# Optimization experiments

Measured on AMD Instinct MI355X. Metric: run time of the kernel, lower is better.

The kernel has to match this reference:

```python
import jax, jax.numpy as jnp
import numpy as np

H = 128          # hidden_size
L = 3            # num_layers
N = 200_000      # total atoms across all fragments
E = 400_000      # bidirectional bonds (avg degree ~2)
G = 8192         # number of molecular subgraphs
ATOM_V = 120
BOND_V = 5


def setup_inputs() -> dict:
    key = jax.random.key(0)
    ks = jax.random.split(key, 14)
    s = 1.0 / np.sqrt(H)
    f = lambda k, shp: (jax.random.normal(k, shp, jnp.float32) * s)
    return {
        "atom_types": jax.random.randint(ks[0], (N,), 0, ATOM_V),
        "edges": jax.random.randint(ks[1], (2, E), 0, N),
        "edge_types": jax.random.randint(ks[2], (E,), 0, BOND_V),
        "node_batch": jnp.sort(jax.random.randint(ks[3], (N,), 0, G)),
        "atom_emb": f(ks[4], (ATOM_V, H)),
        "bond_emb": f(ks[5], (BOND_V, H)),
        "conv_w1": f(ks[6], (L, H, H)),
        "conv_b1": jnp.zeros((L, H), jnp.float32),
        "conv_w2": f(ks[7], (L, H, H)),
        "conv_b2": jnp.zeros((L, H), jnp.float32),
        "proj_w1": f(ks[8], (H, H)),
        "proj_b1": jnp.zeros((H,), jnp.float32),
        "proj_w2": f(ks[9], (H, H)),
        "proj_b2": jnp.zeros((H,), jnp.float32),
    }


def reference(atom_types, edges, edge_types, node_batch,
              atom_emb, bond_emb,
              conv_w1, conv_b1, conv_w2, conv_b2,
              proj_w1, proj_b1, proj_w2, proj_b2):
    # node / bond embeddings (torch clamps indices to vocab-1)
    x = atom_emb[jnp.clip(atom_types, 0, ATOM_V - 1)]       # [N, H]
    a = bond_emb[jnp.clip(edge_types, 0, BOND_V - 1)]       # [E, H]
    src, dst = edges[0], edges[1]
    # GINEConv layers: x_i' = MLP(x_i + sum_{j->i} ReLU(x_j + e_ji)), eps=0
    for l in range(L):
        m = jax.nn.relu(x[src] + a)                         # [E, H] edge messages
        agg = jax.ops.segment_sum(m, dst, num_segments=N)   # scatter-add to dst nodes
        h = x + agg
        h = jax.nn.relu(h @ conv_w1[l] + conv_b1[l])
        x = h @ conv_w2[l] + conv_b2[l]
    # per-graph mean readout
    sums = jax.ops.segment_sum(x, node_batch, num_segments=G)                      # [G, H]
    cnt = jax.ops.segment_sum(jnp.ones((N, 1), x.dtype), node_batch, num_segments=G)
    g = sums / jnp.maximum(cnt, 1.0)
    # proj: Linear -> SiLU -> Linear
    g = jax.nn.silu(g @ proj_w1 + proj_b1)
    return g @ proj_w2 + proj_b2                            # [G, H]
```

## Files before the change

### kernel.cpp

```cpp
#include <hip/hip_runtime.h>

typedef unsigned short u16;
typedef __attribute__((ext_vector_type(8))) short short8;
typedef __attribute__((ext_vector_type(4))) float f32x4;

#define HDIM 128
#define SCAN_B 512
#define CSH 2048
#define PREP_BLOCKS 572

__device__ __forceinline__ float bf2f(u16 v) {
    return __uint_as_float(((unsigned int)v) << 16);
}
__device__ __forceinline__ u16 f2bf(float f) {
    unsigned int u = __float_as_uint(f);
    unsigned int r = (u + 0x7FFFu + ((u >> 16) & 1u)) >> 16;
    return (u16)r;
}

__global__ __launch_bounds__(256) void prep_hist_kernel(
    const float* __restrict__ w1, const float* __restrict__ w2,
    const float* __restrict__ pw1, const float* __restrict__ pw2,
    const float* __restrict__ atom_emb,
    u16* __restrict__ wt, u16* __restrict__ ebf,
    const int* __restrict__ edges, int* __restrict__ deg, int E, int N)
{
    if (blockIdx.x < PREP_BLOCKS) {
        int gid = blockIdx.x * 256 + threadIdx.x;
        if (gid < 8 * 16384) {
            int mat = gid >> 14;
            int idx = gid & 16383;
            int n = idx >> 7, k = idx & 127;
            const float* src;
            if      (mat < 3) src = w1 + mat * 16384;
            else if (mat < 6) src = w2 + (mat - 3) * 16384;
            else if (mat == 6) src = pw1;
            else               src = pw2;
            wt[gid] = f2bf(src[k * 128 + n]);
        } else {
            int i = gid - 8 * 16384;
            ebf[i] = f2bf(atom_emb[i]);
        }
    } else {
        int e = (blockIdx.x - PREP_BLOCKS) * 256 + threadIdx.x;
        if (e >= E) return;
        int d = edges[E + e];
        d = d < 0 ? 0 : (d >= N ? N - 1 : d);
        atomicAdd(&deg[d], 1);
    }
}

__global__ __launch_bounds__(SCAN_B) void scan_block_kernel(
    const int* __restrict__ deg, int* __restrict__ offs, int* __restrict__ bsum, int N)
{
    __shared__ int tmp[SCAN_B];
    int t = threadIdx.x;
    int gid = blockIdx.x * SCAN_B + t;
    int v = (gid < N) ? deg[gid] : 0;
    tmp[t] = v;
    __syncthreads();
#pragma unroll
    for (int off = 1; off < SCAN_B; off <<= 1) {
        int add = (t >= off) ? tmp[t - off] : 0;
        __syncthreads();
        tmp[t] += add;
        __syncthreads();
    }
    if (gid < N) offs[gid] = tmp[t] - v;
    if (t == SCAN_B - 1) bsum[blockIdx.x] = tmp[t];
}

__global__ __launch_bounds__(256) void finalize_offs_kernel(
    int* __restrict__ offs, const int* __restrict__ bsum,
    int* __restrict__ cursor, const int* __restrict__ nb,
    int* __restrict__ gbounds, int N, int E, int G)
{
    __shared__ int red[256];
    const int tid = threadIdx.x;
    const int B = blockIdx.x >> 1;
    int sum = 0;
    for (int t = tid; t < B; t += 256) sum += bsum[t];
    red[tid] = sum;
    __syncthreads();
#pragma unroll
    for (int off = 128; off > 0; off >>= 1) {
        if (tid < off) red[tid] += red[tid + off];
        __syncthreads();
    }
    int prefix = red[0];
    int gid = blockIdx.x * 256 + tid;
    if (gid < N) {
        int v = offs[gid] + prefix;
        offs[gid] = v;
        cursor[gid] = v;
        int cur = nb[gid]; cur = cur < 0 ? 0 : (cur > G - 1 ? G - 1 : cur);
        if (gid == 0) {
            for (int g = 0; g <= cur; g++) gbounds[g] = 0;
        } else {
            int prev = nb[gid - 1]; prev = prev < 0 ? 0 : (prev > G - 1 ? G - 1 : prev);
            for (int g = prev + 1; g <= cur; g++) gbounds[g] = gid;
        }
        if (gid == N - 1) {
            for (int g = cur + 1; g <= G; g++) gbounds[g] = N;
        }
    }
    if (gid == 0) offs[N] = E;
}

__global__ __launch_bounds__(256) void fill_csr_kernel(
    const int* __restrict__ edges, const int* __restrict__ etypes,
    int* __restrict__ cursor, int* __restrict__ csr, int E, int N)
{
    int e = blockIdx.x * 256 + threadIdx.x;
    if (e >= E) return;
    int s = edges[e], d = edges[E + e], t = etypes[e];
    s = s < 0 ? 0 : (s >= N ? N - 1 : s);
    d = d < 0 ? 0 : (d >= N ? N - 1 : d);
    t = t < 0 ? 0 : (t > 4 ? 4 : t);
    int pos = atomicAdd(&cursor[d], 1);
    csr[pos] = (s << 3) | t;
}

__global__ __launch_bounds__(512, 4) void gine_kernel(
    const u16* __restrict__ x_in, u16* __restrict__ x_out,
    const int* __restrict__ types, int use_emb, const u16* __restrict__ ebf,
    const int* __restrict__ offs, const int* __restrict__ csr,
    const float* __restrict__ bond_emb,
    const u16* __restrict__ w1t, const float* __restrict__ b1,
    const u16* __restrict__ w2t, const float* __restrict__ b2, int N)
{
    __shared__ __align__(16) u16 As[128][136];
    __shared__ __align__(16) u16 Ws[128][136];
    __shared__ __align__(16) u16 bsh[5 * 128];
    __shared__ __align__(16) int csh[CSH];
    const int tid  = threadIdx.x;
    const int row0 = blockIdx.x * 128;
    const int wave = tid >> 6, lane = tid & 63;
    const int m = lane & 15, quad = lane >> 4;

    for (int i = tid; i < 640; i += 512) bsh[i] = f2bf(bond_emb[i]);
    {
        const uint4* src = (const uint4*)w1t;
        for (int i = tid; i < 2048; i += 512) {
            int n = i >> 4, k8 = i & 15;
            *(uint4*)&Ws[n][k8 * 8] = src[i];
        }
    }
    const int rend = (row0 + 128 < N) ? row0 + 128 : N;
    const int e0 = offs[row0];
    {
        int cnt = offs[rend] - e0;
        cnt = cnt < CSH ? cnt : CSH;
        for (int i = tid; i < cnt; i += 512) csh[i] = csr[e0 + i];
    }
    {
        const int rp = tid >> 4, c8 = (tid & 15) * 8;
        __syncthreads();

        int rowA = row0 + rp,      rowB = row0 + 32 + rp;
        int rowC = row0 + 64 + rp, rowD = row0 + 96 + rp;
        int rcA = rowA < N ? rowA : N - 1;
        int rcB = rowB < N ? rowB : N - 1;
        int rcC = rowC < N ? rowC : N - 1;
        int rcD = rowD < N ? rowD : N - 1;
        const u16 *spA, *spB, *spC, *spD;
        if (use_emb) {
            int tA = types[rcA]; tA = tA < 0 ? 0 : (tA > 119 ? 119 : tA);
            int tB = types[rcB]; tB = tB < 0 ? 0 : (tB > 119 ? 119 : tB);
            int tC = types[rcC]; tC = tC < 0 ? 0 : (tC > 119 ? 119 : tC);
            int tD = types[rcD]; tD = tD < 0 ? 0 : (tD > 119 ? 119 : tD);
            spA = ebf + (size_t)tA * 128; spB = ebf + (size_t)tB * 128;
            spC = ebf + (size_t)tC * 128; spD = ebf + (size_t)tD * 128;
        } else {
            spA = x_in + (size_t)rcA * 128; spB = x_in + (size_t)rcB * 128;
            spC = x_in + (size_t)rcC * 128; spD = x_in + (size_t)rcD * 128;
        }
        int jbA = offs[rcA], jeA = rowA < N ? offs[rcA + 1] : jbA;
        int jbB = offs[rcB], jeB = rowB < N ? offs[rcB + 1] : jbB;
        int jbC = offs[rcC], jeC = rowC < N ? offs[rcC + 1] : jbC;
        int jbD = offs[rcD], jeD = rowD < N ? offs[rcD + 1] : jbD;
        uint4 svA = *(const uint4*)(spA + c8);
        uint4 svB = *(const uint4*)(spB + c8);
        uint4 svC = *(const uint4*)(spC + c8);
        uint4 svD = *(const uint4*)(spD + c8);
        float accA[8], accB[8], accC[8], accD[8];
        {
            const u16* pA = (const u16*)&svA; const u16* pB = (const u16*)&svB;
            const u16* pC = (const u16*)&svC; const u16* pD = (const u16*)&svD;
#pragma unroll
            for (int i = 0; i < 8; i++) {
                accA[i] = bf2f(pA[i]); accB[i] = bf2f(pB[i]);
                accC[i] = bf2f(pC[i]); accD[i] = bf2f(pD[i]);
            }
        }
        int lbA = jbA - e0, lbB = jbB - e0, lbC = jbC - e0, lbD = jbD - e0;
        int dA = jeA - jbA, dB = jeB - jbB, dC = jeC - jbC, dD = jeD - jbD;
        int dmax = dA > dB ? dA : dB;
        dmax = dC > dmax ? dC : dmax;
        dmax = dD > dmax ? dD : dmax;
        for (int k = 0; k < dmax; k += 2) {
            bool a0 = k < dA,     a1 = (k + 1) < dA;
            bool a2 = k < dB,     a3 = (k + 1) < dB;
            bool a4 = k < dC,     a5 = (k + 1) < dC;
            bool a6 = k < dD,     a7 = (k + 1) < dD;
            int v0 = 0, v1 = 0, v2 = 0, v3 = 0, v4 = 0, v5 = 0, v6 = 0, v7 = 0;
            if (a0) { int li = lbA + k;     v0 = (li < CSH) ? csh[li] : csr[jbA + k]; }
            if (a1) { int li = lbA + k + 1; v1 = (li < CSH) ? csh[li] : csr[jbA + k + 1]; }
            if (a2) { int li = lbB + k;     v2 = (li < CSH) ? csh[li] : csr[jbB + k]; }
            if (a3) { int li = lbB + k + 1; v3 = (li < CSH) ? csh[li] : csr[jbB + k + 1]; }
            if (a4) { int li = lbC + k;     v4 = (li < CSH) ? csh[li] : csr[jbC + k]; }
            if (a5) { int li = lbC + k + 1; v5 = (li < CSH) ? csh[li] : csr[jbC + k + 1]; }
            if (a6) { int li = lbD + k;     v6 = (li < CSH) ? csh[li] : csr[jbD + k]; }
            if (a7) { int li = lbD + k + 1; v7 = (li < CSH) ? csh[li] : csr[jbD + k + 1]; }
            const u16 *p0, *p1, *p2, *p3, *p4, *p5, *p6, *p7;
            if (use_emb) {
                int t0 = types[v0 >> 3]; t0 = t0 < 0 ? 0 : (t0 > 119 ? 119 : t0);
                int t1 = types[v1 >> 3]; t1 = t1 < 0 ? 0 : (t1 > 119 ? 119 : t1);
                int t2 = types[v2 >> 3]; t2 = t2 < 0 ? 0 : (t2 > 119 ? 119 : t2);
                int t3 = types[v3 >> 3]; t3 = t3 < 0 ? 0 : (t3 > 119 ? 119 : t3);
                int t4 = types[v4 >> 3]; t4 = t4 < 0 ? 0 : (t4 > 119 ? 119 : t4);
                int t5 = types[v5 >> 3]; t5 = t5 < 0 ? 0 : (t5 > 119 ? 119 : t5);
                int t6 = types[v6 >> 3]; t6 = t6 < 0 ? 0 : (t6 > 119 ? 119 : t6);
                int t7 = types[v7 >> 3]; t7 = t7 < 0 ? 0 : (t7 > 119 ? 119 : t7);
                p0 = ebf + (size_t)t0 * 128; p1 = ebf + (size_t)t1 * 128;
                p2 = ebf + (size_t)t2 * 128; p3 = ebf + (size_t)t3 * 128;
                p4 = ebf + (size_t)t4 * 128; p5 = ebf + (size_t)t5 * 128;
                p6 = ebf + (size_t)t6 * 128; p7 = ebf + (size_t)t7 * 128;
            } else {
                p0 = x_in + (size_t)(v0 >> 3) * 128; p1 = x_in + (size_t)(v1 >> 3) * 128;
                p2 = x_in + (size_t)(v2 >> 3) * 128; p3 = x_in + (size_t)(v3 >> 3) * 128;
                p4 = x_in + (size_t)(v4 >> 3) * 128; p5 = x_in + (size_t)(v5 >> 3) * 128;
                p6 = x_in + (size_t)(v6 >> 3) * 128; p7 = x_in + (size_t)(v7 >> 3) * 128;
            }
            uint4 g0 = *(const uint4*)(p0 + c8);
            uint4 g1 = *(const uint4*)(p1 + c8);
            uint4 g2 = *(const uint4*)(p2 + c8);
            uint4 g3 = *(const uint4*)(p3 + c8);
            uint4 g4 = *(const uint4*)(p4 + c8);
            uint4 g5 = *(const uint4*)(p5 + c8);
            uint4 g6 = *(const uint4*)(p6 + c8);
            uint4 g7 = *(const uint4*)(p7 + c8);
            if (a0) { const u16* gp = (const u16*)&g0; const u16* bp = bsh + (v0 & 7) * 128 + c8;
#pragma unroll
                for (int i = 0; i < 8; i++) { float mm = bf2f(gp[i]) + bf2f(bp[i]); accA[i] += mm > 0.f ? mm : 0.f; } }
            if (a1) { const u16* gp = (const u16*)&g1; const u16* bp = bsh + (v1 & 7) * 128 + c8;
#pragma unroll
                for (int i = 0; i < 8; i++) { float mm = bf2f(gp[i]) + bf2f(bp[i]); accA[i] += mm > 0.f ? mm : 0.f; } }
            if (a2) { const u16* gp = (const u16*)&g2; const u16* bp = bsh + (v2 & 7) * 128 + c8;
#pragma unroll
                for (int i = 0; i < 8; i++) { float mm = bf2f(gp[i]) + bf2f(bp[i]); accB[i] += mm > 0.f ? mm : 0.f; } }
            if (a3) { const u16* gp = (const u16*)&g3; const u16* bp = bsh + (v3 & 7) * 128 + c8;
#pragma unroll
                for (int i = 0; i < 8; i++) { float mm = bf2f(gp[i]) + bf2f(bp[i]); accB[i] += mm > 0.f ? mm : 0.f; } }
            if (a4) { const u16* gp = (const u16*)&g4; const u16* bp = bsh + (v4 & 7) * 128 + c8;
#pragma unroll
                for (int i = 0; i < 8; i++) { float mm = bf2f(gp[i]) + bf2f(bp[i]); accC[i] += mm > 0.f ? mm : 0.f; } }
            if (a5) { const u16* gp = (const u16*)&g5; const u16* bp = bsh + (v5 & 7) * 128 + c8;
#pragma unroll
                for (int i = 0; i < 8; i++) { float mm = bf2f(gp[i]) + bf2f(bp[i]); accC[i] += mm > 0.f ? mm : 0.f; } }
            if (a6) { const u16* gp = (const u16*)&g6; const u16* bp = bsh + (v6 & 7) * 128 + c8;
#pragma unroll
                for (int i = 0; i < 8; i++) { float mm = bf2f(gp[i]) + bf2f(bp[i]); accD[i] += mm > 0.f ? mm : 0.f; } }
            if (a7) { const u16* gp = (const u16*)&g7; const u16* bp = bsh + (v7 & 7) * 128 + c8;
#pragma unroll
                for (int i = 0; i < 8; i++) { float mm = bf2f(gp[i]) + bf2f(bp[i]); accD[i] += mm > 0.f ? mm : 0.f; } }
        }
        uint4 ovA = make_uint4(0u,0u,0u,0u), ovB = ovA, ovC = ovA, ovD = ovA;
        if (rowA < N) { u16* op = (u16*)&ovA;
#pragma unroll
            for (int i = 0; i < 8; i++) op[i] = f2bf(accA[i]); }
        if (rowB < N) { u16* op = (u16*)&ovB;
#pragma unroll
            for (int i = 0; i < 8; i++) op[i] = f2bf(accB[i]); }
        if (rowC < N) { u16* op = (u16*)&ovC;
#pragma unroll
            for (int i = 0; i < 8; i++) op[i] = f2bf(accC[i]); }
        if (rowD < N) { u16* op = (u16*)&ovD;
#pragma unroll
            for (int i = 0; i < 8; i++) op[i] = f2bf(accD[i]); }
        *(uint4*)&As[rp][c8]      = ovA;
        *(uint4*)&As[32 + rp][c8] = ovB;
        *(uint4*)&As[64 + rp][c8] = ovC;
        *(uint4*)&As[96 + rp][c8] = ovD;
    }
    __syncthreads();

    f32x4 acc[8];
#pragma unroll
    for (int c = 0; c < 8; c++) acc[c] = (f32x4){0.f, 0.f, 0.f, 0.f};
#pragma unroll
    for (int q = 0; q < 4; q++) {
        short8 a = *(const short8*)&As[wave * 16 + m][q * 32 + quad * 8];
#pragma unroll
        for (int c = 0; c < 8; c++) {
            short8 b = *(const short8*)&Ws[c * 16 + m][q * 32 + quad * 8];
            acc[c] = __builtin_amdgcn_mfma_f32_16x16x32_bf16(a, b, acc[c], 0, 0, 0);
        }
    }
    __syncthreads();
    {
        const uint4* src = (const uint4*)w2t;
        for (int i = tid; i < 2048; i += 512) {
            int n = i >> 4, k8 = i & 15;
            *(uint4*)&Ws[n][k8 * 8] = src[i];
        }
    }
#pragma unroll
    for (int c = 0; c < 8; c++) {
        int col = c * 16 + m;
        float bias = b1[col];
#pragma unroll
        for (int r = 0; r < 4; r++) {
            float v = acc[c][r] + bias;
            v = v > 0.f ? v : 0.f;
            As[wave * 16 + quad * 4 + r][col] = f2bf(v);
        }
    }
    __syncthreads();
    f32x4 acc2[8];
#pragma unroll
    for (int c = 0; c < 8; c++) acc2[c] = (f32x4){0.f, 0.f, 0.f, 0.f};
#pragma unroll
    for (int q = 0; q < 4; q++) {
        short8 a = *(const short8*)&As[wave * 16 + m][q * 32 + quad * 8];
#pragma unroll
        for (int c = 0; c < 8; c++) {
            short8 b = *(const short8*)&Ws[c * 16 + m][q * 32 + quad * 8];
            acc2[c] = __builtin_amdgcn_mfma_f32_16x16x32_bf16(a, b, acc2[c], 0, 0, 0);
        }
    }
    __syncthreads();
#pragma unroll
    for (int c = 0; c < 8; c++) {
        int col = c * 16 + m;
        float bias = b2[col];
#pragma unroll
        for (int r = 0; r < 4; r++)
            As[wave * 16 + quad * 4 + r][col] = f2bf(acc2[c][r] + bias);
    }
    __syncthreads();
    for (int i = tid; i < 2048; i += 512) {
        int r = i >> 4, c8 = (i & 15) * 8;
        int row = row0 + r;
        if (row < N) *(uint4*)(x_out + (size_t)row * 128 + c8) = *(const uint4*)&As[r][c8];
    }
}

__global__ __launch_bounds__(256) void readout_mean_kernel(
    const u16* __restrict__ x, const int* __restrict__ gbounds,
    u16* __restrict__ gm, int N)
{
    __shared__ float part[16][128];
    int b = blockIdx.x;
    int tid = threadIdx.x;
    int s = gbounds[b], e = gbounds[b + 1];
    int rg = tid >> 4, c8 = (tid & 15) * 8;
    float acc[8];
#pragma unroll
    for (int i = 0; i < 8; i++) acc[i] = 0.f;
    for (int n = s + rg; n < e; n += 16) {
        uint4 v = *(const uint4*)(x + (size_t)n * 128 + c8);
        const u16* vp = (const u16*)&v;
#pragma unroll
        for (int i = 0; i < 8; i++) acc[i] += bf2f(vp[i]);
    }
#pragma unroll
    for (int i = 0; i < 8; i++) part[rg][c8 + i] = acc[i];
    __syncthreads();
    if (tid < 128) {
        float sum = 0.f;
#pragma unroll
        for (int g = 0; g < 16; g++) sum += part[g][tid];
        float cnt = (float)((e - s) > 0 ? (e - s) : 1);
        gm[(size_t)b * 128 + tid] = f2bf(sum / cnt);
    }
}

__global__ __launch_bounds__(256) void proj_kernel(
    const u16* __restrict__ gm, float* __restrict__ out,
    const u16* __restrict__ pw1t, const float* __restrict__ pb1,
    const u16* __restrict__ pw2t, const float* __restrict__ pb2, int G)
{
    __shared__ __align__(16) u16 As[64][136];
    __shared__ __align__(16) u16 Ws[128][136];
    const int tid  = threadIdx.x;
    const int row0 = blockIdx.x * 64;
    const int wave = tid >> 6, lane = tid & 63;
    const int m = lane & 15, quad = lane >> 4;

    {
        const uint4* src = (const uint4*)pw1t;
        for (int i = tid; i < 2048; i += 256) {
            int n = i >> 4, k8 = i & 15;
            *(uint4*)&Ws[n][k8 * 8] = src[i];
        }
    }
    for (int i = tid; i < 1024; i += 256) {
        int r = i >> 4, c8 = (i & 15) * 8;
        int row = row0 + r;
        uint4 ov = make_uint4(0u, 0u, 0u, 0u);
        if (row < G) ov = *(const uint4*)(gm + (size_t)row * 128 + c8);
        *(uint4*)&As[r][c8] = ov;
    }
    __syncthreads();
    f32x4 acc[8];
#pragma unroll
    for (int c = 0; c < 8; c++) acc[c] = (f32x4){0.f, 0.f, 0.f, 0.f};
#pragma unroll
    for (int q = 0; q < 4; q++) {
        short8 a = *(const short8*)&As[wave * 16 + m][q * 32 + quad * 8];
#pragma unroll
        for (int c = 0; c < 8; c++) {
            short8 b = *(const short8*)&Ws[c * 16 + m][q * 32 + quad * 8];
            acc[c] = __builtin_amdgcn_mfma_f32_16x16x32_bf16(a, b, acc[c], 0, 0, 0);
        }
    }
    __syncthreads();
    {
        const uint4* src = (const uint4*)pw2t;
        for (int i = tid; i < 2048; i += 256) {
            int n = i >> 4, k8 = i & 15;
            *(uint4*)&Ws[n][k8 * 8] = src[i];
        }
    }
#pragma unroll
    for (int c = 0; c < 8; c++) {
        int col = c * 16 + m;
        float bias = pb1[col];
#pragma unroll
        for (int r = 0; r < 4; r++) {
            float v = acc[c][r] + bias;
            v = v / (1.f + __expf(-v));
            As[wave * 16 + quad * 4 + r][col] = f2bf(v);
        }
    }
    __syncthreads();
    f32x4 acc2[8];
#pragma unroll
    for (int c = 0; c < 8; c++) acc2[c] = (f32x4){0.f, 0.f, 0.f, 0.f};
#pragma unroll
    for (int q = 0; q < 4; q++) {
        short8 a = *(const short8*)&As[wave * 16 + m][q * 32 + quad * 8];
#pragma unroll
        for (int c = 0; c < 8; c++) {
            short8 b = *(const short8*)&Ws[c * 16 + m][q * 32 + quad * 8];
            acc2[c] = __builtin_amdgcn_mfma_f32_16x16x32_bf16(a, b, acc2[c], 0, 0, 0);
        }
    }
#pragma unroll
    for (int c = 0; c < 8; c++) {
        int col = c * 16 + m;
        float bias = pb2[col];
#pragma unroll
        for (int r = 0; r < 4; r++) {
            int row = row0 + wave * 16 + quad * 4 + r;
            if (row < G) out[(size_t)row * 128 + col] = acc2[c][r] + bias;
        }
    }
}

extern "C" void kernel_launch(void* const* d_in, const int* in_sizes, int n_in,
                              void* d_out, int out_size, void* d_ws, size_t ws_size,
                              hipStream_t stream) {
    const int*   atom_types  = (const int*)d_in[0];
    const int*   edges       = (const int*)d_in[1];
    const int*   edge_types  = (const int*)d_in[2];
    const int*   node_batch  = (const int*)d_in[3];
    const float* atom_emb    = (const float*)d_in[4];
    const float* bond_emb    = (const float*)d_in[5];
    const float* conv_w1     = (const float*)d_in[6];
    const float* conv_b1     = (const float*)d_in[7];
    const float* conv_w2     = (const float*)d_in[8];
    const float* conv_b2     = (const float*)d_in[9];
    const float* pw1         = (const float*)d_in[10];
    const float* pb1         = (const float*)d_in[11];
    const float* pw2         = (const float*)d_in[12];
    const float* pb2         = (const float*)d_in[13];
    float* out = (float*)d_out;

    const int N = in_sizes[0];
    const int E = in_sizes[2];
    const int G = out_size / HDIM;
    const int nblk = (N + SCAN_B - 1) / SCAN_B;

    size_t xA_bytes  = (size_t)N * HDIM * sizeof(u16);
    size_t xB_bytes  = (size_t)N * HDIM * sizeof(u16);
    size_t wt_bytes  = (size_t)8 * HDIM * HDIM * sizeof(u16);
    size_t ebf_bytes = (size_t)120 * HDIM * sizeof(u16);
    size_t gm_bytes  = (size_t)G * HDIM * sizeof(u16);
    size_t deg_bytes = (size_t)N * 4;
    size_t off_bytes = (size_t)(N + 1) * 4;
    size_t cur_bytes = (size_t)N * 4;
    size_t bs_bytes  = (size_t)nblk * 4;
    size_t gb_bytes  = (size_t)(G + 1) * 4;
    size_t csr_bytes = (size_t)E * 4;
    size_t need = xA_bytes + xB_bytes + wt_bytes + ebf_bytes + gm_bytes +
                  deg_bytes + off_bytes + cur_bytes + bs_bytes + gb_bytes + csr_bytes;
    if (ws_size < need) {
        hipMemsetAsync(d_out, 0, (size_t)out_size * sizeof(float), stream);
        return;
    }
    char* p = (char*)d_ws;
    u16* xA     = (u16*)p;  p += xA_bytes;
    u16* xB     = (u16*)p;  p += xB_bytes;
    u16* wt     = (u16*)p;  p += wt_bytes;
    u16* ebf    = (u16*)p;  p += ebf_bytes;
    u16* gm     = (u16*)p;  p += gm_bytes;
    int* deg    = (int*)p;  p += deg_bytes;
    int* offs   = (int*)p;  p += off_bytes;
    int* cur    = (int*)p;  p += cur_bytes;
    int* bsum   = (int*)p;  p += bs_bytes;
    int* gbound = (int*)p;  p += gb_bytes;
    int* csr    = (int*)p;

    hipMemsetAsync(deg, 0, deg_bytes, stream);
    prep_hist_kernel<<<PREP_BLOCKS + (E + 255) / 256, 256, 0, stream>>>(
        conv_w1, conv_w2, pw1, pw2, atom_emb, wt, ebf, edges, deg, E, N);
    scan_block_kernel<<<nblk, SCAN_B, 0, stream>>>(deg, offs, bsum, N);
    finalize_offs_kernel<<<(N + 255) / 256, 256, 0, stream>>>(
        offs, bsum, cur, node_batch, gbound, N, E, G);
    fill_csr_kernel<<<(E + 255) / 256, 256, 0, stream>>>(edges, edge_types, cur, csr, E, N);

    const int gblocks = (N + 127) / 128;
    gine_kernel<<<gblocks, 512, 0, stream>>>(
        xB , xA, atom_types, 1, ebf, offs, csr, bond_emb,
        wt + 0 * 16384, conv_b1 + 0, wt + 3 * 16384, conv_b2 + 0, N);
    gine_kernel<<<gblocks, 512, 0, stream>>>(
        xA, xB, atom_types, 0, ebf, offs, csr, bond_emb,
        wt + 1 * 16384, conv_b1 + 128, wt + 4 * 16384, conv_b2 + 128, N);
    gine_kernel<<<gblocks, 512, 0, stream>>>(
        xB, xA, atom_types, 0, ebf, offs, csr, bond_emb,
        wt + 2 * 16384, conv_b1 + 256, wt + 5 * 16384, conv_b2 + 256, N);

    readout_mean_kernel<<<G, 256, 0, stream>>>(xA, gbound, gm, N);
    proj_kernel<<<(G + 63) / 64, 256, 0, stream>>>(
        gm, out, wt + 6 * 16384, pb1, wt + 7 * 16384, pb2, G);
}
```

Baseline: 342.4 us.

## Split fused GINE layer into separate aggregation and MLP kernels

The fused gather+MLP kernel is split into an aggregation kernel with small shared memory and launch bounds allowing 8 blocks per CU, plus a separate MFMA MLP kernel that reloads the aggregated rows from global memory. The shared-memory staging of the CSR slice is also dropped, so neighbour indices are read straight from global memory. The aim is higher occupancy for the latency-bound gather phase. In exchange there are extra kernel launches and an extra write and read of an N×128 bf16 intermediate per layer.

New measurement: 570.9 us. 66.7% more time.

```diff
diff --git a/kernel.cpp b/kernel.cpp
--- a/kernel.cpp
+++ b/kernel.cpp
@@ -6,7 +6,6 @@
 
 #define HDIM 128
 #define SCAN_B 512
-#define CSH 2048
 #define PREP_BLOCKS 572
 
 __device__ __forceinline__ float bf2f(u16 v) {
@@ -121,24 +120,155 @@
     csr[pos] = (s << 3) | t;
 }
 
-__global__ __launch_bounds__(512, 4) void gine_kernel(
-    const u16* __restrict__ x_in, u16* __restrict__ x_out,
+__global__ __launch_bounds__(512, 8) void agg_kernel(
+    const u16* __restrict__ x_in, u16* __restrict__ xa,
     const int* __restrict__ types, int use_emb, const u16* __restrict__ ebf,
     const int* __restrict__ offs, const int* __restrict__ csr,
-    const float* __restrict__ bond_emb,
+    const float* __restrict__ bond_emb, int N)
+{
+    __shared__ __align__(16) u16 bsh[5 * 128];
+    const int tid  = threadIdx.x;
+    const int row0 = blockIdx.x * 128;
+    for (int i = tid; i < 640; i += 512) bsh[i] = f2bf(bond_emb[i]);
+    const int rp = tid >> 4, c8 = (tid & 15) * 8;
+    __syncthreads();
+
+    int rowA = row0 + rp,      rowB = row0 + 32 + rp;
+    int rowC = row0 + 64 + rp, rowD = row0 + 96 + rp;
+    int rcA = rowA < N ? rowA : N - 1;
+    int rcB = rowB < N ? rowB : N - 1;
+    int rcC = rowC < N ? rowC : N - 1;
+    int rcD = rowD < N ? rowD : N - 1;
+    const u16 *spA, *spB, *spC, *spD;
+    if (use_emb) {
+        int tA = types[rcA]; tA = tA < 0 ? 0 : (tA > 119 ? 119 : tA);
+        int tB = types[rcB]; tB = tB < 0 ? 0 : (tB > 119 ? 119 : tB);
+        int tC = types[rcC]; tC = tC < 0 ? 0 : (tC > 119 ? 119 : tC);
+        int tD = types[rcD]; tD = tD < 0 ? 0 : (tD > 119 ? 119 : tD);
+        spA = ebf + (size_t)tA * 128; spB = ebf + (size_t)tB * 128;
+        spC = ebf + (size_t)tC * 128; spD = ebf + (size_t)tD * 128;
+    } else {
+        spA = x_in + (size_t)rcA * 128; spB = x_in + (size_t)rcB * 128;
+        spC = x_in + (size_t)rcC * 128; spD = x_in + (size_t)rcD * 128;
+    }
+    int jbA = offs[rcA], jeA = rowA < N ? offs[rcA + 1] : jbA;
+    int jbB = offs[rcB], jeB = rowB < N ? offs[rcB + 1] : jbB;
+    int jbC = offs[rcC], jeC = rowC < N ? offs[rcC + 1] : jbC;
+    int jbD = offs[rcD], jeD = rowD < N ? offs[rcD + 1] : jbD;
+    uint4 svA = *(const uint4*)(spA + c8);
+    uint4 svB = *(const uint4*)(spB + c8);
+    uint4 svC = *(const uint4*)(spC + c8);
+    uint4 svD = *(const uint4*)(spD + c8);
+    float accA[8], accB[8], accC[8], accD[8];
+    {
+        const u16* pA = (const u16*)&svA; const u16* pB = (const u16*)&svB;
+        const u16* pC = (const u16*)&svC; const u16* pD = (const u16*)&svD;
+#pragma unroll
+        for (int i = 0; i < 8; i++) {
+            accA[i] = bf2f(pA[i]); accB[i] = bf2f(pB[i]);
+            accC[i] = bf2f(pC[i]); accD[i] = bf2f(pD[i]);
+        }
+    }
+    int dA = jeA - jbA, dB = jeB - jbB, dC = jeC - jbC, dD = jeD - jbD;
+    int dmax = dA > dB ? dA : dB;
+    dmax = dC > dmax ? dC : dmax;
+    dmax = dD > dmax ? dD : dmax;
+    for (int k = 0; k < dmax; k += 2) {
+        bool a0 = k < dA,     a1 = (k + 1) < dA;
+        bool a2 = k < dB,     a3 = (k + 1) < dB;
+        bool a4 = k < dC,     a5 = (k + 1) < dC;
+        bool a6 = k < dD,     a7 = (k + 1) < dD;
+        int v0 = a0 ? csr[jbA + k] : 0;  int v1 = a1 ? csr[jbA + k + 1] : 0;
+        int v2 = a2 ? csr[jbB + k] : 0;  int v3 = a3 ? csr[jbB + k + 1] : 0;
+        int v4 = a4 ? csr[jbC + k] : 0;  int v5 = a5 ? csr[jbC + k + 1] : 0;
+        int v6 = a6 ? csr[jbD + k] : 0;  int v7 = a7 ? csr[jbD + k + 1] : 0;
+        const u16 *p0, *p1, *p2, *p3, *p4, *p5, *p6, *p7;
+        if (use_emb) {
+            int t0 = types[v0 >> 3]; t0 = t0 < 0 ? 0 : (t0 > 119 ? 119 : t0);
+            int t1 = types[v1 >> 3]; t1 = t1 < 0 ? 0 : (t1 > 119 ? 119 : t1);
+            int t2 = types[v2 >> 3]; t2 = t2 < 0 ? 0 : (t2 > 119 ? 119 : t2);
+            int t3 = types[v3 >> 3]; t3 = t3 < 0 ? 0 : (t3 > 119 ? 119 : t3);
+            int t4 = types[v4 >> 3]; t4 = t4 < 0 ? 0 : (t4 > 119 ? 119 : t4);
+            int t5 = types[v5 >> 3]; t5 = t5 < 0 ? 0 : (t5 > 119 ? 119 : t5);
+            int t6 = types[v6 >> 3]; t6 = t6 < 0 ? 0 : (t6 > 119 ? 119 : t6);
+            int t7 = types[v7 >> 3]; t7 = t7 < 0 ? 0 : (t7 > 119 ? 119 : t7);
+            p0 = ebf + (size_t)t0 * 128; p1 = ebf + (size_t)t1 * 128;
+            p2 = ebf + (size_t)t2 * 128; p3 = ebf + (size_t)t3 * 128;
+            p4 = ebf + (size_t)t4 * 128; p5 = ebf + (size_t)t5 * 128;
+            p6 = ebf + (size_t)t6 * 128; p7 = ebf + (size_t)t7 * 128;
+        } else {
+            p0 = x_in + (size_t)(v0 >> 3) * 128; p1 = x_in + (size_t)(v1 >> 3) * 128;
+            p2 = x_in + (size_t)(v2 >> 3) * 128; p3 = x_in + (size_t)(v3 >> 3) * 128;
+            p4 = x_in + (size_t)(v4 >> 3) * 128; p5 = x_in + (size_t)(v5 >> 3) * 128;
+            p6 = x_in + (size_t)(v6 >> 3) * 128; p7 = x_in + (size_t)(v7 >> 3) * 128;
+        }
+        uint4 g0 = *(const uint4*)(p0 + c8);
+        uint4 g1 = *(const uint4*)(p1 + c8);
+        uint4 g2 = *(const uint4*)(p2 + c8);
+        uint4 g3 = *(const uint4*)(p3 + c8);
+        uint4 g4 = *(const uint4*)(p4 + c8);
+        uint4 g5 = *(const uint4*)(p5 + c8);
+        uint4 g6 = *(const uint4*)(p6 + c8);
+        uint4 g7 = *(const uint4*)(p7 + c8);
+        if (a0) { const u16* gp = (const u16*)&g0; const u16* bp = bsh + (v0 & 7) * 128 + c8;
+#pragma unroll
+            for (int i = 0; i < 8; i++) { float mm = bf2f(gp[i]) + bf2f(bp[i]); accA[i] += mm > 0.f ? mm : 0.f; } }
+        if (a1) { const u16* gp = (const u16*)&g1; const u16* bp = bsh + (v1 & 7) * 128 + c8;
+#pragma unroll
+            for (int i = 0; i < 8; i++) { float mm = bf2f(gp[i]) + bf2f(bp[i]); accA[i] += mm > 0.f ? mm : 0.f; } }
+        if (a2) { const u16* gp = (const u16*)&g2; const u16* bp = bsh + (v2 & 7) * 128 + c8;
+#pragma unroll
+            for (int i = 0; i < 8; i++) { float mm = bf2f(gp[i]) + bf2f(bp[i]); accB[i] += mm > 0.f ? mm : 0.f; } }
+        if (a3) { const u16* gp = (const u16*)&g3; const u16* bp = bsh + (v3 & 7) * 128 + c8;
+#pragma unroll
+            for (int i = 0; i < 8; i++) { float mm = bf2f(gp[i]) + bf2f(bp[i]); accB[i] += mm > 0.f ? mm : 0.f; } }
+        if (a4) { const u16* gp = (const u16*)&g4; const u16* bp = bsh + (v4 & 7) * 128 + c8;
+#pragma unroll
+            for (int i = 0; i < 8; i++) { float mm = bf2f(gp[i]) + bf2f(bp[i]); accC[i] += mm > 0.f ? mm : 0.f; } }
+        if (a5) { const u16* gp = (const u16*)&g5; const u16* bp = bsh + (v5 & 7) * 128 + c8;
+#pragma unroll
+            for (int i = 0; i < 8; i++) { float mm = bf2f(gp[i]) + bf2f(bp[i]); accC[i] += mm > 0.f ? mm : 0.f; } }
+        if (a6) { const u16* gp = (const u16*)&g6; const u16* bp = bsh + (v6 & 7) * 128 + c8;
+#pragma unroll
+            for (int i = 0; i < 8; i++) { float mm = bf2f(gp[i]) + bf2f(bp[i]); accD[i] += mm > 0.f ? mm : 0.f; } }
+        if (a7) { const u16* gp = (const u16*)&g7; const u16* bp = bsh + (v7 & 7) * 128 + c8;
+#pragma unroll
+            for (int i = 0; i < 8; i++) { float mm = bf2f(gp[i]) + bf2f(bp[i]); accD[i] += mm > 0.f ? mm : 0.f; } }
+    }
+    uint4 ovA, ovB, ovC, ovD;
+    {
+        u16* op;
+        op = (u16*)&ovA;
+#pragma unroll
+        for (int i = 0; i < 8; i++) op[i] = f2bf(accA[i]);
+        op = (u16*)&ovB;
+#pragma unroll
+        for (int i = 0; i < 8; i++) op[i] = f2bf(accB[i]);
+        op = (u16*)&ovC;
+#pragma unroll
+        for (int i = 0; i < 8; i++) op[i] = f2bf(accC[i]);
+        op = (u16*)&ovD;
+#pragma unroll
+        for (int i = 0; i < 8; i++) op[i] = f2bf(accD[i]);
+    }
+    if (rowA < N) *(uint4*)(xa + (size_t)rowA * 128 + c8) = ovA;
+    if (rowB < N) *(uint4*)(xa + (size_t)rowB * 128 + c8) = ovB;
+    if (rowC < N) *(uint4*)(xa + (size_t)rowC * 128 + c8) = ovC;
+    if (rowD < N) *(uint4*)(xa + (size_t)rowD * 128 + c8) = ovD;
+}
+
+__global__ __launch_bounds__(512, 4) void mlp_kernel(
+    const u16* __restrict__ xa, u16* __restrict__ x_out,
     const u16* __restrict__ w1t, const float* __restrict__ b1,
     const u16* __restrict__ w2t, const float* __restrict__ b2, int N)
 {
     __shared__ __align__(16) u16 As[128][136];
     __shared__ __align__(16) u16 Ws[128][136];
-    __shared__ __align__(16) u16 bsh[5 * 128];
-    __shared__ __align__(16) int csh[CSH];
     const int tid  = threadIdx.x;
     const int row0 = blockIdx.x * 128;
     const int wave = tid >> 6, lane = tid & 63;
     const int m = lane & 15, quad = lane >> 4;
 
-    for (int i = tid; i < 640; i += 512) bsh[i] = f2bf(bond_emb[i]);
     {
         const uint4* src = (const uint4*)w1t;
         for (int i = tid; i < 2048; i += 512) {
@@ -146,142 +276,12 @@
             *(uint4*)&Ws[n][k8 * 8] = src[i];
         }
     }
-    const int rend = (row0 + 128 < N) ? row0 + 128 : N;
-    const int e0 = offs[row0];
-    {
-        int cnt = offs[rend] - e0;
-        cnt = cnt < CSH ? cnt : CSH;
-        for (int i = tid; i < cnt; i += 512) csh[i] = csr[e0 + i];
-    }
-    {
-        const int rp = tid >> 4, c8 = (tid & 15) * 8;
-        __syncthreads();
-
-        int rowA = row0 + rp,      rowB = row0 + 32 + rp;
-        int rowC = row0 + 64 + rp, rowD = row0 + 96 + rp;
-        int rcA = rowA < N ? rowA : N - 1;
-        int rcB = rowB < N ? rowB : N - 1;
-        int rcC = rowC < N ? rowC : N - 1;
-        int rcD = rowD < N ? rowD : N - 1;
-        const u16 *spA, *spB, *spC, *spD;
-        if (use_emb) {
-            int tA = types[rcA]; tA = tA < 0 ? 0 : (tA > 119 ? 119 : tA);
-            int tB = types[rcB]; tB = tB < 0 ? 0 : (tB > 119 ? 119 : tB);
-            int tC = types[rcC]; tC = tC < 0 ? 0 : (tC > 119 ? 119 : tC);
-            int tD = types[rcD]; tD = tD < 0 ? 0 : (tD > 119 ? 119 : tD);
-            spA = ebf + (size_t)tA * 128; spB = ebf + (size_t)tB * 128;
-            spC = ebf + (size_t)tC * 128; spD = ebf + (size_t)tD * 128;
-        } else {
-            spA = x_in + (size_t)rcA * 128; spB = x_in + (size_t)rcB * 128;
-            spC = x_in + (size_t)rcC * 128; spD = x_in + (size_t)rcD * 128;
-        }
-        int jbA = offs[rcA], jeA = rowA < N ? offs[rcA + 1] : jbA;
-        int jbB = offs[rcB], jeB = rowB < N ? offs[rcB + 1] : jbB;
-        int jbC = offs[rcC], jeC = rowC < N ? offs[rcC + 1] : jbC;
-        int jbD = offs[rcD], jeD = rowD < N ? offs[rcD + 1] : jbD;
-        uint4 svA = *(const uint4*)(spA + c8);
-        uint4 svB = *(const uint4*)(spB + c8);
-        uint4 svC = *(const uint4*)(spC + c8);
-        uint4 svD = *(const uint4*)(spD + c8);
-        float accA[8], accB[8], accC[8], accD[8];
-        {
-            const u16* pA = (const u16*)&svA; const u16* pB = (const u16*)&svB;
-            const u16* pC = (const u16*)&svC; const u16* pD = (const u16*)&svD;
-#pragma unroll
-            for (int i = 0; i < 8; i++) {
-                accA[i] = bf2f(pA[i]); accB[i] = bf2f(pB[i]);
-                accC[i] = bf2f(pC[i]); accD[i] = bf2f(pD[i]);
-            }
-        }
-        int lbA = jbA - e0, lbB = jbB - e0, lbC = jbC - e0, lbD = jbD - e0;
-        int dA = jeA - jbA, dB = jeB - jbB, dC = jeC - jbC, dD = jeD - jbD;
-        int dmax = dA > dB ? dA : dB;
-        dmax = dC > dmax ? dC : dmax;
-        dmax = dD > dmax ? dD : dmax;
-        for (int k = 0; k < dmax; k += 2) {
-            bool a0 = k < dA,     a1 = (k + 1) < dA;
-            bool a2 = k < dB,     a3 = (k + 1) < dB;
-            bool a4 = k < dC,     a5 = (k + 1) < dC;
-            bool a6 = k < dD,     a7 = (k + 1) < dD;
-            int v0 = 0, v1 = 0, v2 = 0, v3 = 0, v4 = 0, v5 = 0, v6 = 0, v7 = 0;
-            if (a0) { int li = lbA + k;     v0 = (li < CSH) ? csh[li] : csr[jbA + k]; }
-            if (a1) { int li = lbA + k + 1; v1 = (li < CSH) ? csh[li] : csr[jbA + k + 1]; }
-            if (a2) { int li = lbB + k;     v2 = (li < CSH) ? csh[li] : csr[jbB + k]; }
-            if (a3) { int li = lbB + k + 1; v3 = (li < CSH) ? csh[li] : csr[jbB + k + 1]; }
-            if (a4) { int li = lbC + k;     v4 = (li < CSH) ? csh[li] : csr[jbC + k]; }
-            if (a5) { int li = lbC + k + 1; v5 = (li < CSH) ? csh[li] : csr[jbC + k + 1]; }
-            if (a6) { int li = lbD + k;     v6 = (li < CSH) ? csh[li] : csr[jbD + k]; }
-            if (a7) { int li = lbD + k + 1; v7 = (li < CSH) ? csh[li] : csr[jbD + k + 1]; }
-            const u16 *p0, *p1, *p2, *p3, *p4, *p5, *p6, *p7;
-            if (use_emb) {
-                int t0 = types[v0 >> 3]; t0 = t0 < 0 ? 0 : (t0 > 119 ? 119 : t0);
-                int t1 = types[v1 >> 3]; t1 = t1 < 0 ? 0 : (t1 > 119 ? 119 : t1);
-                int t2 = types[v2 >> 3]; t2 = t2 < 0 ? 0 : (t2 > 119 ? 119 : t2);
-                int t3 = types[v3 >> 3]; t3 = t3 < 0 ? 0 : (t3 > 119 ? 119 : t3);
-                int t4 = types[v4 >> 3]; t4 = t4 < 0 ? 0 : (t4 > 119 ? 119 : t4);
-                int t5 = types[v5 >> 3]; t5 = t5 < 0 ? 0 : (t5 > 119 ? 119 : t5);
-                int t6 = types[v6 >> 3]; t6 = t6 < 0 ? 0 : (t6 > 119 ? 119 : t6);
-                int t7 = types[v7 >> 3]; t7 = t7 < 0 ? 0 : (t7 > 119 ? 119 : t7);
-                p0 = ebf + (size_t)t0 * 128; p1 = ebf + (size_t)t1 * 128;
-                p2 = ebf + (size_t)t2 * 128; p3 = ebf + (size_t)t3 * 128;
-                p4 = ebf + (size_t)t4 * 128; p5 = ebf + (size_t)t5 * 128;
-                p6 = ebf + (size_t)t6 * 128; p7 = ebf + (size_t)t7 * 128;
-            } else {
-                p0 = x_in + (size_t)(v0 >> 3) * 128; p1 = x_in + (size_t)(v1 >> 3) * 128;
-                p2 = x_in + (size_t)(v2 >> 3) * 128; p3 = x_in + (size_t)(v3 >> 3) * 128;
-                p4 = x_in + (size_t)(v4 >> 3) * 128; p5 = x_in + (size_t)(v5 >> 3) * 128;
-                p6 = x_in + (size_t)(v6 >> 3) * 128; p7 = x_in + (size_t)(v7 >> 3) * 128;
-            }
-            uint4 g0 = *(const uint4*)(p0 + c8);
-            uint4 g1 = *(const uint4*)(p1 + c8);
-            uint4 g2 = *(const uint4*)(p2 + c8);
-            uint4 g3 = *(const uint4*)(p3 + c8);
-            uint4 g4 = *(const uint4*)(p4 + c8);
-            uint4 g5 = *(const uint4*)(p5 + c8);
-            uint4 g6 = *(const uint4*)(p6 + c8);
-            uint4 g7 = *(const uint4*)(p7 + c8);
-            if (a0) { const u16* gp = (const u16*)&g0; const u16* bp = bsh + (v0 & 7) * 128 + c8;
-#pragma unroll
-                for (int i = 0; i < 8; i++) { float mm = bf2f(gp[i]) + bf2f(bp[i]); accA[i] += mm > 0.f ? mm : 0.f; } }
-            if (a1) { const u16* gp = (const u16*)&g1; const u16* bp = bsh + (v1 & 7) * 128 + c8;
-#pragma unroll
-                for (int i = 0; i < 8; i++) { float mm = bf2f(gp[i]) + bf2f(bp[i]); accA[i] += mm > 0.f ? mm : 0.f; } }
-            if (a2) { const u16* gp = (const u16*)&g2; const u16* bp = bsh + (v2 & 7) * 128 + c8;
-#pragma unroll
-                for (int i = 0; i < 8; i++) { float mm = bf2f(gp[i]) + bf2f(bp[i]); accB[i] += mm > 0.f ? mm : 0.f; } }
-            if (a3) { const u16* gp = (const u16*)&g3; const u16* bp = bsh + (v3 & 7) * 128 + c8;
-#pragma unroll
-                for (int i = 0; i < 8; i++) { float mm = bf2f(gp[i]) + bf2f(bp[i]); accB[i] += mm > 0.f ? mm : 0.f; } }
-            if (a4) { const u16* gp = (const u16*)&g4; const u16* bp = bsh + (v4 & 7) * 128 + c8;
-#pragma unroll
-                for (int i = 0; i < 8; i++) { float mm = bf2f(gp[i]) + bf2f(bp[i]); accC[i] += mm > 0.f ? mm : 0.f; } }
-            if (a5) { const u16* gp = (const u16*)&g5; const u16* bp = bsh + (v5 & 7) * 128 + c8;
-#pragma unroll
-                for (int i = 0; i < 8; i++) { float mm = bf2f(gp[i]) + bf2f(bp[i]); accC[i] += mm > 0.f ? mm : 0.f; } }
-            if (a6) { const u16* gp = (const u16*)&g6; const u16* bp = bsh + (v6 & 7) * 128 + c8;
-#pragma unroll
-                for (int i = 0; i < 8; i++) { float mm = bf2f(gp[i]) + bf2f(bp[i]); accD[i] += mm > 0.f ? mm : 0.f; } }
-            if (a7) { const u16* gp = (const u16*)&g7; const u16* bp = bsh + (v7 & 7) * 128 + c8;
-#pragma unroll
-                for (int i = 0; i < 8; i++) { float mm = bf2f(gp[i]) + bf2f(bp[i]); accD[i] += mm > 0.f ? mm : 0.f; } }
-        }
-        uint4 ovA = make_uint4(0u,0u,0u,0u), ovB = ovA, ovC = ovA, ovD = ovA;
-        if (rowA < N) { u16* op = (u16*)&ovA;
-#pragma unroll
-            for (int i = 0; i < 8; i++) op[i] = f2bf(accA[i]); }
-        if (rowB < N) { u16* op = (u16*)&ovB;
-#pragma unroll
-            for (int i = 0; i < 8; i++) op[i] = f2bf(accB[i]); }
-        if (rowC < N) { u16* op = (u16*)&ovC;
-#pragma unroll
-            for (int i = 0; i < 8; i++) op[i] = f2bf(accC[i]); }
-        if (rowD < N) { u16* op = (u16*)&ovD;
-#pragma unroll
-            for (int i = 0; i < 8; i++) op[i] = f2bf(accD[i]); }
-        *(uint4*)&As[rp][c8]      = ovA;
-        *(uint4*)&As[32 + rp][c8] = ovB;
-        *(uint4*)&As[64 + rp][c8] = ovC;
-        *(uint4*)&As[96 + rp][c8] = ovD;
+    for (int i = tid; i < 2048; i += 512) {
+        int r = i >> 4, c8 = (i & 15) * 8;
+        int row = row0 + r;
+        uint4 ov = make_uint4(0u, 0u, 0u, 0u);
+        if (row < N) ov = *(const uint4*)(xa + (size_t)row * 128 + c8);
+        *(uint4*)&As[r][c8] = ov;
     }
     __syncthreads();
 
@@ -522,15 +522,18 @@
     fill_csr_kernel<<<(E + 255) / 256, 256, 0, stream>>>(edges, edge_types, cur, csr, E, N);
 
     const int gblocks = (N + 127) / 128;
-    gine_kernel<<<gblocks, 512, 0, stream>>>(
-        xB , xA, atom_types, 1, ebf, offs, csr, bond_emb,
-        wt + 0 * 16384, conv_b1 + 0, wt + 3 * 16384, conv_b2 + 0, N);
-    gine_kernel<<<gblocks, 512, 0, stream>>>(
-        xA, xB, atom_types, 0, ebf, offs, csr, bond_emb,
-        wt + 1 * 16384, conv_b1 + 128, wt + 4 * 16384, conv_b2 + 128, N);
-    gine_kernel<<<gblocks, 512, 0, stream>>>(
-        xB, xA, atom_types, 0, ebf, offs, csr, bond_emb,
-        wt + 2 * 16384, conv_b1 + 256, wt + 5 * 16384, conv_b2 + 256, N);
+    agg_kernel<<<gblocks, 512, 0, stream>>>(
+        xA , xB, atom_types, 1, ebf, offs, csr, bond_emb, N);
+    mlp_kernel<<<gblocks, 512, 0, stream>>>(
+        xB, xA, wt + 0 * 16384, conv_b1 + 0, wt + 3 * 16384, conv_b2 + 0, N);
+    agg_kernel<<<gblocks, 512, 0, stream>>>(
+        xA, xB, atom_types, 0, ebf, offs, csr, bond_emb, N);
+    mlp_kernel<<<gblocks, 512, 0, stream>>>(
+        xB, xA, wt + 1 * 16384, conv_b1 + 128, wt + 4 * 16384, conv_b2 + 128, N);
+    agg_kernel<<<gblocks, 512, 0, stream>>>(
+        xA, xB, atom_types, 0, ebf, offs, csr, bond_emb, N);
+    mlp_kernel<<<gblocks, 512, 0, stream>>>(
+        xB, xA, wt + 2 * 16384, conv_b1 + 256, wt + 5 * 16384, conv_b2 + 256, N);
 
     readout_mean_kernel<<<G, 256, 0, stream>>>(xA, gbound, gm, N);
     proj_kernel<<<(G + 63) / 64, 256, 0, stream>>>(
```
